# Performance work log

Measured on AMD Instinct MI355X. Metric: run time of the kernel, lower is better.

## Reference

```python
import jax, jax.numpy as jnp
import numpy as np

BATCH, D_MODEL, N_STATE, SEQ_L = 8, 1024, 64, 2048


def setup_inputs() -> dict:
    key = jax.random.key(0)
    k_u, k_a, k_b, k_c = jax.random.split(key, 4)
    scale = 1.0 / (D_MODEL * N_STATE) ** 0.5
    u = jax.random.normal(k_u, (BATCH, D_MODEL, SEQ_L), dtype=jnp.float32)
    # A is stored as a full NxN diagonal matrix, as in the torch module
    A = jnp.diag(jax.random.uniform(k_a, (N_STATE,), dtype=jnp.float32))
    B = jax.random.normal(k_b, (D_MODEL, N_STATE), dtype=jnp.float32) * scale
    C = jax.random.normal(k_c, (D_MODEL, N_STATE), dtype=jnp.float32) * scale
    return {"L": SEQ_L, "u": u, "A": A, "B": B, "C": C}


def reference(L, u, A, B, C):
    # u: (B, D, L). einsum('nn,bnd->bnd', A, h) in torch == diag(A) broadcast over h.
    a = jnp.diagonal(A)                       # (N,)
    Bu = jnp.einsum('dn,bdl->bnl', B, u)      # (B, N, L)
    Cu = jnp.einsum('dn,bdl->bnl', C, u)      # (B, N, L)
    bsz, d, _ = u.shape
    h0 = jnp.zeros((bsz, a.shape[0], d), dtype=u.dtype)  # (B, N, D)

    def step(h, xs):
        bu_l, cu_l, u_l = xs                  # (B,N), (B,N), (B,D)
        h = a[None, :, None] * h + bu_l[:, :, None] * u_l[:, None, :]
        y_l = jnp.einsum('bn,bnd->bd', cu_l, h)
        return h, y_l

    xs = (jnp.moveaxis(Bu, -1, 0), jnp.moveaxis(Cu, -1, 0), jnp.moveaxis(u, -1, 0))
    _, ys = jax.lax.scan(step, h0, xs)        # ys: (L, B, D)
    return jnp.moveaxis(ys, 0, -1)            # (B, D, L)
```

## Files before the change

kernel.cpp:

```cpp
#include <hip/hip_runtime.h>
#include <hip/hip_bf16.h>
#include <string.h>

#define BATCH 8
#define DM 1024
#define NS 64
#define SL 2048
#define NC 32
#define TC 64

typedef __attribute__((ext_vector_type(8))) short bf16x8;
typedef __attribute__((ext_vector_type(4))) float f32x4;
typedef float v2f __attribute__((ext_vector_type(2)));

__device__ inline unsigned short f2bf(float f) {
    union { float f; unsigned u; } v; v.f = f;
    return (unsigned short)((v.u + 0x7fffu + ((v.u >> 16) & 1u)) >> 16);
}
__device__ inline float bf2f(unsigned short h) {
    return __uint_as_float(((unsigned)h) << 16);
}
static __device__ inline v2f bfpair_to_v2f(unsigned int p) {
    unsigned int lo = p << 16, hi = p & 0xffff0000u;
    v2f r; r.x = __uint_as_float(lo); r.y = __uint_as_float(hi); return r;
}


__global__ __launch_bounds__(256) void k_prep(const float* __restrict__ Bm,
                                              const float* __restrict__ Cm,
                                              unsigned short* __restrict__ BT,
                                              unsigned short* __restrict__ CT)
{
    __shared__ float sT[64][65];
    const float* src = blockIdx.y ? Cm : Bm;
    unsigned short* dst = blockIdx.y ? CT : BT;
    const int d0 = blockIdx.x * 64, t = threadIdx.x;
    {
        int r = t >> 2, f = (t & 3) * 16;
#pragma unroll
        for (int i = 0; i < 4; i++) {
            float4 v = *(const float4*)&src[(size_t)(d0 + r) * NS + f + i * 4];
            sT[r][f + i * 4 + 0] = v.x; sT[r][f + i * 4 + 1] = v.y;
            sT[r][f + i * 4 + 2] = v.z; sT[r][f + i * 4 + 3] = v.w;
        }
    }
    __syncthreads();
    {
        int n = t >> 2, dq = (t & 3) * 16;
        unsigned pk[8];
#pragma unroll
        for (int k = 0; k < 8; k++) {
            unsigned short a = f2bf(sT[dq + 2 * k][n]);
            unsigned short bb = f2bf(sT[dq + 2 * k + 1][n]);
            pk[k] = (unsigned)a | ((unsigned)bb << 16);
        }
        uint4 v0 = { pk[0], pk[1], pk[2], pk[3] };
        uint4 v1 = { pk[4], pk[5], pk[6], pk[7] };
        *(uint4*)&dst[(size_t)n * DM + d0 + dq] = v0;
        *(uint4*)&dst[(size_t)n * DM + d0 + dq + 8] = v1;
    }
}

__global__ __launch_bounds__(512) void k_proj(const float* __restrict__ u,
                                              const unsigned short* __restrict__ BC,
                                              unsigned short* __restrict__ BuT,
                                              unsigned short* __restrict__ CuT,
                                              unsigned short* __restrict__ Ubf)
{
    __shared__ unsigned short sA[32 * 64];
    __shared__ unsigned short sB[128 * 64];
    const int b = blockIdx.y, l0 = blockIdx.x * 32, t = threadIdx.x;
    const int lane = t & 63, w = t >> 6, g = lane >> 4, m15 = lane & 15;
    const int dd = t >> 3, c8 = t & 7;
    const int dq = dd >> 3, d7 = dd & 7;

    f32x4 acc[2];
    acc[0] = (f32x4){0.f, 0.f, 0.f, 0.f};
    acc[1] = (f32x4){0.f, 0.f, 0.f, 0.f};

#pragma unroll 1
    for (int d0 = 0; d0 < DM; d0 += 64) {
        __syncthreads();
        {
            float4 v = *(const float4*)&u[((size_t)b * DM + d0 + dd) * SL + l0 + c8 * 4];
            unsigned short b0 = f2bf(v.x), b1 = f2bf(v.y), b2 = f2bf(v.z), b3 = f2bf(v.w);
            int l = c8 * 4;
            sA[(l + 0) * 64 + ((dq ^ ((l + 0) & 7)) * 8) + d7] = b0;
            sA[(l + 1) * 64 + ((dq ^ ((l + 1) & 7)) * 8) + d7] = b1;
            sA[(l + 2) * 64 + ((dq ^ ((l + 2) & 7)) * 8) + d7] = b2;
            sA[(l + 3) * 64 + ((dq ^ ((l + 3) & 7)) * 8) + d7] = b3;
            uint2 pk = { (unsigned)b0 | ((unsigned)b1 << 16),
                         (unsigned)b2 | ((unsigned)b3 << 16) };
            *(uint2*)(Ubf + ((size_t)b * DM + d0 + dd) * SL + l0 + c8 * 4) = pk;
        }
#pragma unroll
        for (int p = 0; p < 2; p++) {
            int idx = p * 512 + t;
            int row = idx >> 3, cc8 = idx & 7;
            uint4 v = *(const uint4*)(BC + (size_t)row * DM + d0 + cc8 * 8);
            *(uint4*)&sB[row * 64 + ((cc8 ^ (row & 7)) * 8)] = v;
        }
        __syncthreads();
#pragma unroll
        for (int ks = 0; ks < 2; ks++) {
            bf16x8 af[2], bfr;
#pragma unroll
            for (int mt = 0; mt < 2; mt++) {
                int r = mt * 16 + m15;
                af[mt] = *(const bf16x8*)&sA[r * 64 + (((ks * 4 + g) ^ (r & 7)) * 8)];
            }
            {
                int r = w * 16 + m15;
                bfr = *(const bf16x8*)&sB[r * 64 + (((ks * 4 + g) ^ (r & 7)) * 8)];
            }
#pragma unroll
            for (int mt = 0; mt < 2; mt++)
                acc[mt] = __builtin_amdgcn_mfma_f32_16x16x32_bf16(af[mt], bfr, acc[mt], 0, 0, 0);
        }
    }
    {
        int wn = w * 16 + m15;
        unsigned short* dst = (wn < 64) ? BuT : CuT;
        int n = wn & 63;
#pragma unroll
        for (int mt = 0; mt < 2; mt++)
#pragma unroll
            for (int r = 0; r < 4; r++) {
                int l = l0 + mt * 16 + g * 4 + r;
                dst[((size_t)b * SL + l) * NS + n] = f2bf(acc[mt][r]);
            }
    }
}

__global__ __launch_bounds__(256) void k_g(const float* __restrict__ A,
                                           const unsigned short* __restrict__ BuT,
                                           const unsigned short* __restrict__ CuT,
                                           unsigned short* __restrict__ Gw,
                                           unsigned short* __restrict__ Bvw,
                                           unsigned short* __restrict__ Wcw)
{
    __shared__ unsigned short sCu[64 * 64];
    __shared__ unsigned short sBu[8 * 64 * 8];
    __shared__ unsigned short sP[8 * 66 * 8];
    __shared__ unsigned short sTb[64 * 66];
    const int cc = blockIdx.x, b = cc >> 5, c = cc & 31;
    const int gy = blockIdx.y;
    const int t = threadIdx.x, lane = t & 63;
    const int l0 = c * TC;
    const size_t gbase = (size_t)cc * 4096;

    {
        const unsigned short* srcC = CuT + ((size_t)b * SL + l0) * NS;
        const unsigned short* srcB = BuT + ((size_t)b * SL + l0) * NS;
#pragma unroll
        for (int p = 0; p < 2; p++) {
            int idx = p * 256 + t;
            int r = idx >> 3, q8 = idx & 7;
            uint4 vc = *(const uint4*)(srcC + (size_t)r * NS + q8 * 8);
            *(uint4*)&sCu[r * 64 + q8 * 8] = vc;
            uint4 vb = *(const uint4*)(srcB + (size_t)r * NS + q8 * 8);
            *(uint4*)&sBu[(q8 * 64 + r) * 8] = vb;
        }
    }
    {
        int n = t & 63;
        float an = A[n * NS + n];
        int q = n >> 3, n7 = n & 7;
#pragma unroll 1
        for (int dl = (t >> 6) * 17; dl < (t >> 6) * 17 + 17 && dl <= 64; dl++)
            sP[(q * 66 + dl) * 8 + n7] = f2bf(__powf(an, (float)dl));
    }
    __syncthreads();

#pragma unroll 1
    for (int r = gy * 8; r < gy * 8 + 8; r++) {
        int idx = r * 256 + t;
        int l = idx >> 6;
        int lp = lane;
        int dl = l - lp;
        float acc = 0.f;
        if (dl >= 0) {
#pragma unroll
            for (int q = 0; q < 8; q++) {
                bf16x8 cu = *(const bf16x8*)&sCu[l * 64 + q * 8];
                bf16x8 bu = *(const bf16x8*)&sBu[(q * 64 + lp) * 8];
                bf16x8 pp = *(const bf16x8*)&sP[(q * 66 + dl) * 8];
#pragma unroll
                for (int j = 0; j < 8; j++)
                    acc = fmaf(bf2f((unsigned short)cu[j]) * bf2f((unsigned short)bu[j]),
                               bf2f((unsigned short)pp[j]), acc);
            }
        }
        Gw[gbase + l * 64 + lp] = (dl >= 0) ? f2bf(acc) : (unsigned short)0;
    }

    if (gy == 0) {
#pragma unroll 1
        for (int r = 0; r < 16; r++) {
            int idx = r * 256 + t;
            int l = idx >> 6;
            int n = lane, q = n >> 3, n7 = n & 7;
            float cu = bf2f(sCu[l * 64 + n]);
            float pv = bf2f(sP[(q * 66 + (l + 1)) * 8 + n7]);
            Wcw[gbase + l * 64 + n] = f2bf(cu * pv);
        }
    } else {
#pragma unroll 1
        for (int r = 0; r < 16; r++) {
            int idx = r * 256 + t;
            int l = idx >> 6;
            int n = lane, q = n >> 3, n7 = n & 7;
            float bu = bf2f(sBu[(q * 64 + l) * 8 + n7]);
            float pv = bf2f(sP[(q * 66 + (63 - l)) * 8 + n7]);
            sTb[n * 66 + l] = f2bf(bu * pv);
        }
        __syncthreads();
#pragma unroll 1
        for (int r = 0; r < 16; r++) {
            int idx = r * 256 + t;
            int n = idx >> 6;
            int l = lane;
            Bvw[gbase + n * 64 + l] = sTb[n * 66 + l];
        }
    }
}

__global__ __launch_bounds__(256) void k_state(const unsigned short* __restrict__ Ubf,
                                               const unsigned short* __restrict__ Bvw,
                                               unsigned short* __restrict__ Ew)
{
    __shared__ unsigned short sV[64 * 64];
    const int slab = blockIdx.x, c = blockIdx.y, b = blockIdx.z;
    const int d0 = slab * 128, l0 = c * TC;
    const int t = threadIdx.x, lane = t & 63, w = t >> 6, g = lane >> 4, m15 = lane & 15;

    {
        size_t gbase = ((size_t)(b * NC + c)) * 4096;
        int rr = t >> 3, c8 = t & 7;
#pragma unroll
        for (int p = 0; p < 2; p++) {
            int r = p * 32 + rr;
            uint4 vv = *(const uint4*)(Bvw + gbase + r * 64 + c8 * 8);
            *(uint4*)&sV[r * 64 + ((c8 ^ (r & 7)) * 8)] = vv;
        }
    }
    __syncthreads();

    const unsigned short* ub = Ubf + ((size_t)b * DM + d0) * SL + l0;

    f32x4 accE[2][4];
#pragma unroll
    for (int i = 0; i < 2; i++)
#pragma unroll
        for (int j = 0; j < 4; j++) accE[i][j] = (f32x4){0.f, 0.f, 0.f, 0.f};

#pragma unroll
    for (int ks = 0; ks < 2; ks++) {
        int kq = ks * 4 + g;
        bf16x8 af[2];
#pragma unroll
        for (int mt = 0; mt < 2; mt++) {
            int r = w * 32 + mt * 16 + m15;
            af[mt] = *(const bf16x8*)(ub + (size_t)r * SL + kq * 8);
        }
#pragma unroll
        for (int nt = 0; nt < 4; nt++) {
            int rg = nt * 16 + m15;
            bf16x8 bv = *(const bf16x8*)&sV[rg * 64 + ((kq ^ (rg & 7)) * 8)];
#pragma unroll
            for (int mt = 0; mt < 2; mt++)
                accE[mt][nt] = __builtin_amdgcn_mfma_f32_16x16x32_bf16(af[mt], bv, accE[mt][nt], 0, 0, 0);
        }
    }
#pragma unroll
    for (int mt = 0; mt < 2; mt++)
#pragma unroll
        for (int nt = 0; nt < 4; nt++)
#pragma unroll
            for (int r = 0; r < 4; r++) {
                int d = d0 + w * 32 + mt * 16 + g * 4 + r;
                Ew[(((size_t)b * NC + c) * DM + d) * NS + nt * 16 + m15] = f2bf(accE[mt][nt][r]);
            }
}

__global__ __launch_bounds__(256) void k_prefix(const float* __restrict__ A,
                                                unsigned short* __restrict__ E)
{
    int gg = blockIdx.x * 256 + threadIdx.x;
    int p  = gg & 31;
    int d  = (gg >> 5) & (DM - 1);
    int b  = gg >> 15;
    int n0 = p * 2;

    float a0 = A[n0 * NS + n0];
    float a1 = A[(n0 + 1) * NS + (n0 + 1)];
    v2f aT = { __powf(a0, (float)TC), __powf(a1, (float)TC) };
    v2f hs = { 0.f, 0.f };

    unsigned int* base = (unsigned int*)E + ((((size_t)b * NC) * DM + d) * NS >> 1) + p;
    const size_t cstride = ((size_t)DM * NS) >> 1;

#pragma unroll 4
    for (int c = 0; c < NC; c++) {
        unsigned int* ptr = base + (size_t)c * cstride;
        unsigned int e = *ptr;
        unsigned int sw = (unsigned)f2bf(hs.x) | ((unsigned)f2bf(hs.y) << 16);
        *ptr = sw;
        hs = __builtin_elementwise_fma(aT, hs, bfpair_to_v2f(e));
    }
}

__global__ __launch_bounds__(256) void k_y(const unsigned short* __restrict__ Ubf,
                                           const unsigned short* __restrict__ Gw,
                                           const unsigned short* __restrict__ Wcw,
                                           const unsigned short* __restrict__ HS,
                                           float* __restrict__ y)
{
    __shared__ unsigned short sG[64 * 64];
    __shared__ unsigned short sW[64 * 64];
    const int slab = blockIdx.x, c = blockIdx.y, b = blockIdx.z;
    const int d0 = slab * 128, l0 = c * TC;
    const int t = threadIdx.x, lane = t & 63, w = t >> 6, g = lane >> 4, m15 = lane & 15;

    {
        size_t gbase = ((size_t)(b * NC + c)) * 4096;
        int rr = t >> 3, c8 = t & 7;
#pragma unroll
        for (int p = 0; p < 2; p++) {
            int r = p * 32 + rr;
            uint4 gv = *(const uint4*)(Gw + gbase + r * 64 + c8 * 8);
            *(uint4*)&sG[r * 64 + ((c8 ^ (r & 7)) * 8)] = gv;
            uint4 wv = *(const uint4*)(Wcw + gbase + r * 64 + c8 * 8);
            *(uint4*)&sW[r * 64 + ((c8 ^ (r & 7)) * 8)] = wv;
        }
    }
    __syncthreads();

    const unsigned short* ub    = Ubf + ((size_t)b * DM + d0) * SL + l0;
    const unsigned short* hbase = HS + (((size_t)b * NC + c) * DM + d0) * NS;

    f32x4 acc[2][4];
#pragma unroll
    for (int i = 0; i < 2; i++)
#pragma unroll
        for (int j = 0; j < 4; j++) acc[i][j] = (f32x4){0.f, 0.f, 0.f, 0.f};

#pragma unroll
    for (int ks = 0; ks < 2; ks++) {
        int kq = ks * 4 + g;
        bf16x8 af[2];
#pragma unroll
        for (int mt = 0; mt < 2; mt++) {
            int r = w * 32 + mt * 16 + m15;
            af[mt] = *(const bf16x8*)(ub + (size_t)r * SL + kq * 8);
        }
#pragma unroll
        for (int nt = 0; nt < 4; nt++) {
            int rg = nt * 16 + m15;
            bf16x8 bg = *(const bf16x8*)&sG[rg * 64 + ((kq ^ (rg & 7)) * 8)];
#pragma unroll
            for (int mt = 0; mt < 2; mt++)
                acc[mt][nt] = __builtin_amdgcn_mfma_f32_16x16x32_bf16(af[mt], bg, acc[mt][nt], 0, 0, 0);
        }
    }
#pragma unroll
    for (int ks = 0; ks < 2; ks++) {
        int kq = ks * 4 + g;
        bf16x8 ah[2];
#pragma unroll
        for (int mt = 0; mt < 2; mt++) {
            int r = w * 32 + mt * 16 + m15;
            ah[mt] = *(const bf16x8*)(hbase + (size_t)r * NS + kq * 8);
        }
#pragma unroll
        for (int nt = 0; nt < 4; nt++) {
            int rg = nt * 16 + m15;
            bf16x8 bw = *(const bf16x8*)&sW[rg * 64 + ((kq ^ (rg & 7)) * 8)];
#pragma unroll
            for (int mt = 0; mt < 2; mt++)
                acc[mt][nt] = __builtin_amdgcn_mfma_f32_16x16x32_bf16(ah[mt], bw, acc[mt][nt], 0, 0, 0);
        }
    }
#pragma unroll
    for (int mt = 0; mt < 2; mt++)
#pragma unroll
        for (int nt = 0; nt < 4; nt++)
#pragma unroll
            for (int r = 0; r < 4; r++) {
                int d = d0 + w * 32 + mt * 16 + g * 4 + r;
                int l = l0 + nt * 16 + m15;
                y[((size_t)b * DM + d) * SL + l] = acc[mt][nt][r];
            }
}

extern "C" void kernel_launch(void* const* d_in, const int* in_sizes, int n_in,
                              void* d_out, int out_size, void* d_ws, size_t ws_size,
                              hipStream_t stream) {
    const float* u = (const float*)d_in[1];
    const float* A = (const float*)d_in[2];
    const float* B = (const float*)d_in[3];
    const float* C = (const float*)d_in[4];
    float* y = (float*)d_out;

    char* base = (char*)d_ws;
    unsigned short* BuT = (unsigned short*)(base);
    unsigned short* CuT = (unsigned short*)(base + (2u << 20));
    unsigned short* BT  = (unsigned short*)(base + (4u << 20));
    unsigned short* Gw  = (unsigned short*)(base + (5u << 20));
    unsigned short* Bvw = (unsigned short*)(base + (7u << 20));
    unsigned short* Wcw = (unsigned short*)(base + (9u << 20));
    unsigned short* Ew  = (unsigned short*)(base + (11u << 20));
    unsigned short* Ubf = (unsigned short*)(base + (44u << 20));
    unsigned short* CT  = BT + (size_t)NS * DM;

    k_prep<<<dim3(DM / 64, 2), 256, 0, stream>>>(B, C, BT, CT);
    k_proj<<<dim3(SL / 32, BATCH), 512, 0, stream>>>(u, BT, BuT, CuT, Ubf);
    k_g<<<dim3(BATCH * NC, 2), 256, 0, stream>>>(A, BuT, CuT, Gw, Bvw, Wcw);
    k_state<<<dim3(8, NC, BATCH), 256, 0, stream>>>(Ubf, Bvw, Ew);
    k_prefix<<<dim3(BATCH * DM * 32 / 256), 256, 0, stream>>>(A, Ew);
    k_y<<<dim3(8, NC, BATCH), 256, 0, stream>>>(Ubf, Gw, Wcw, Ew, y);
}
```

Baseline: 108.1 us.

## Split k_proj reduction over D into two halves with fp32 partials

The projection kernel now splits the 1024-wide D reduction across two blocks along a new grid z dimension. Each block writes fp32 partial sums to a workspace buffer, and k_g adds the two partials before rounding to bf16. This doubles the number of blocks for the projection GEMM (512 to 1024) to fill more CUs and shortens each block's serial loop. In exchange it adds more intermediate traffic (fp32 and two copies) and a larger workspace layout.

```diff
diff --git a/kernel.cpp b/kernel.cpp
--- a/kernel.cpp
+++ b/kernel.cpp
@@ -63,13 +63,12 @@
 
 __global__ __launch_bounds__(512) void k_proj(const float* __restrict__ u,
                                               const unsigned short* __restrict__ BC,
-                                              unsigned short* __restrict__ BuT,
-                                              unsigned short* __restrict__ CuT,
+                                              float* __restrict__ P,
                                               unsigned short* __restrict__ Ubf)
 {
     __shared__ unsigned short sA[32 * 64];
     __shared__ unsigned short sB[128 * 64];
-    const int b = blockIdx.y, l0 = blockIdx.x * 32, t = threadIdx.x;
+    const int b = blockIdx.y, l0 = blockIdx.x * 32, kk = blockIdx.z, t = threadIdx.x;
     const int lane = t & 63, w = t >> 6, g = lane >> 4, m15 = lane & 15;
     const int dd = t >> 3, c8 = t & 7;
     const int dq = dd >> 3, d7 = dd & 7;
@@ -79,7 +78,8 @@
     acc[1] = (f32x4){0.f, 0.f, 0.f, 0.f};
 
 #pragma unroll 1
-    for (int d0 = 0; d0 < DM; d0 += 64) {
+    for (int it = 0; it < 8; it++) {
+        const int d0 = (kk << 9) + it * 64;
         __syncthreads();
         {
             float4 v = *(const float4*)&u[((size_t)b * DM + d0 + dd) * SL + l0 + c8 * 4];
@@ -120,21 +120,19 @@
     }
     {
         int wn = w * 16 + m15;
-        unsigned short* dst = (wn < 64) ? BuT : CuT;
-        int n = wn & 63;
+        float* dst = P + ((size_t)(kk * BATCH + b) * SL) * 128;
 #pragma unroll
         for (int mt = 0; mt < 2; mt++)
 #pragma unroll
             for (int r = 0; r < 4; r++) {
                 int l = l0 + mt * 16 + g * 4 + r;
-                dst[((size_t)b * SL + l) * NS + n] = f2bf(acc[mt][r]);
+                dst[(size_t)l * 128 + wn] = acc[mt][r];
             }
     }
 }
 
 __global__ __launch_bounds__(256) void k_g(const float* __restrict__ A,
-                                           const unsigned short* __restrict__ BuT,
-                                           const unsigned short* __restrict__ CuT,
+                                           const float* __restrict__ P,
                                            unsigned short* __restrict__ Gw,
                                            unsigned short* __restrict__ Bvw,
                                            unsigned short* __restrict__ Wcw)
@@ -150,16 +148,34 @@
     const size_t gbase = (size_t)cc * 4096;
 
     {
-        const unsigned short* srcC = CuT + ((size_t)b * SL + l0) * NS;
-        const unsigned short* srcB = BuT + ((size_t)b * SL + l0) * NS;
+        const float* p0 = P + ((size_t)b * SL + l0) * 128;
+        const float* p1 = P + ((size_t)(BATCH + b) * SL + l0) * 128;
 #pragma unroll
         for (int p = 0; p < 2; p++) {
             int idx = p * 256 + t;
             int r = idx >> 3, q8 = idx & 7;
-            uint4 vc = *(const uint4*)(srcC + (size_t)r * NS + q8 * 8);
+            const float* r0 = p0 + (size_t)r * 128;
+            const float* r1 = p1 + (size_t)r * 128;
+            float4 a0 = *(const float4*)&r0[q8 * 8];
+            float4 a1 = *(const float4*)&r0[q8 * 8 + 4];
+            float4 b0 = *(const float4*)&r1[q8 * 8];
+            float4 b1 = *(const float4*)&r1[q8 * 8 + 4];
+            uint4 vb;
+            vb.x = (unsigned)f2bf(a0.x + b0.x) | ((unsigned)f2bf(a0.y + b0.y) << 16);
+            vb.y = (unsigned)f2bf(a0.z + b0.z) | ((unsigned)f2bf(a0.w + b0.w) << 16);
+            vb.z = (unsigned)f2bf(a1.x + b1.x) | ((unsigned)f2bf(a1.y + b1.y) << 16);
+            vb.w = (unsigned)f2bf(a1.z + b1.z) | ((unsigned)f2bf(a1.w + b1.w) << 16);
+            *(uint4*)&sBu[(q8 * 64 + r) * 8] = vb;
+            float4 c0 = *(const float4*)&r0[64 + q8 * 8];
+            float4 c1 = *(const float4*)&r0[64 + q8 * 8 + 4];
+            float4 d0v = *(const float4*)&r1[64 + q8 * 8];
+            float4 d1v = *(const float4*)&r1[64 + q8 * 8 + 4];
+            uint4 vc;
+            vc.x = (unsigned)f2bf(c0.x + d0v.x) | ((unsigned)f2bf(c0.y + d0v.y) << 16);
+            vc.y = (unsigned)f2bf(c0.z + d0v.z) | ((unsigned)f2bf(c0.w + d0v.w) << 16);
+            vc.z = (unsigned)f2bf(c1.x + d1v.x) | ((unsigned)f2bf(c1.y + d1v.y) << 16);
+            vc.w = (unsigned)f2bf(c1.z + d1v.z) | ((unsigned)f2bf(c1.w + d1v.w) << 16);
             *(uint4*)&sCu[r * 64 + q8 * 8] = vc;
-            uint4 vb = *(const uint4*)(srcB + (size_t)r * NS + q8 * 8);
-            *(uint4*)&sBu[(q8 * 64 + r) * 8] = vb;
         }
     }
     {
@@ -403,19 +419,18 @@
     float* y = (float*)d_out;
 
     char* base = (char*)d_ws;
-    unsigned short* BuT = (unsigned short*)(base);
-    unsigned short* CuT = (unsigned short*)(base + (2u << 20));
-    unsigned short* BT  = (unsigned short*)(base + (4u << 20));
-    unsigned short* Gw  = (unsigned short*)(base + (5u << 20));
-    unsigned short* Bvw = (unsigned short*)(base + (7u << 20));
-    unsigned short* Wcw = (unsigned short*)(base + (9u << 20));
-    unsigned short* Ew  = (unsigned short*)(base + (11u << 20));
-    unsigned short* Ubf = (unsigned short*)(base + (44u << 20));
+    float*          Pp  = (float*)(base);
+    unsigned short* BT  = (unsigned short*)(base + (16u << 20));
+    unsigned short* Gw  = (unsigned short*)(base + (17u << 20));
+    unsigned short* Bvw = (unsigned short*)(base + (19u << 20));
+    unsigned short* Wcw = (unsigned short*)(base + (21u << 20));
+    unsigned short* Ew  = (unsigned short*)(base + (24u << 20));
+    unsigned short* Ubf = (unsigned short*)(base + (56u << 20));
     unsigned short* CT  = BT + (size_t)NS * DM;
 
     k_prep<<<dim3(DM / 64, 2), 256, 0, stream>>>(B, C, BT, CT);
-    k_proj<<<dim3(SL / 32, BATCH), 512, 0, stream>>>(u, BT, BuT, CuT, Ubf);
-    k_g<<<dim3(BATCH * NC, 2), 256, 0, stream>>>(A, BuT, CuT, Gw, Bvw, Wcw);
+    k_proj<<<dim3(SL / 32, BATCH, 2), 512, 0, stream>>>(u, BT, Pp, Ubf);
+    k_g<<<dim3(BATCH * NC, 2), 256, 0, stream>>>(A, Pp, Gw, Bvw, Wcw);
     k_state<<<dim3(8, NC, BATCH), 256, 0, stream>>>(Ubf, Bvw, Ew);
     k_prefix<<<dim3(BATCH * DM * 32 / 256), 256, 0, stream>>>(A, Ew);
     k_y<<<dim3(8, NC, BATCH), 256, 0, stream>>>(Ubf, Gw, Wcw, Ew, y);
```

After: 111.6 us. 3.3% more time.

## Split-K the projection GEMM into fp32 partials reduced in k_g

Applied to the files above, without the earlier changes.

The projection kernel now splits the D_MODEL reduction into four slices across a new grid dimension. Each block uses 256 threads with a 2x2 MFMA tile per wave and writes fp32 partial sums to a workspace buffer. The consumer kernel k_g sums the four partials and converts them to bf16 when loading its chunk. This trades a shorter serial K-loop and more blocks for an extra 32 MB fp32 partial buffer that is written and read back.

```diff
diff --git a/kernel.cpp b/kernel.cpp
--- a/kernel.cpp
+++ b/kernel.cpp
@@ -8,6 +8,7 @@
 #define SL 2048
 #define NC 32
 #define TC 64
+#define KK 4
 
 typedef __attribute__((ext_vector_type(8))) short bf16x8;
 typedef __attribute__((ext_vector_type(4))) float f32x4;
@@ -61,27 +62,31 @@
     }
 }
 
-__global__ __launch_bounds__(512) void k_proj(const float* __restrict__ u,
+__global__ __launch_bounds__(256) void k_proj(const float* __restrict__ u,
                                               const unsigned short* __restrict__ BC,
-                                              unsigned short* __restrict__ BuT,
-                                              unsigned short* __restrict__ CuT,
+                                              float* __restrict__ P,
                                               unsigned short* __restrict__ Ubf)
 {
     __shared__ unsigned short sA[32 * 64];
     __shared__ unsigned short sB[128 * 64];
-    const int b = blockIdx.y, l0 = blockIdx.x * 32, t = threadIdx.x;
+    const int b = blockIdx.y, l0 = blockIdx.x * 32, kk = blockIdx.z, t = threadIdx.x;
     const int lane = t & 63, w = t >> 6, g = lane >> 4, m15 = lane & 15;
-    const int dd = t >> 3, c8 = t & 7;
-    const int dq = dd >> 3, d7 = dd & 7;
-
-    f32x4 acc[2];
-    acc[0] = (f32x4){0.f, 0.f, 0.f, 0.f};
-    acc[1] = (f32x4){0.f, 0.f, 0.f, 0.f};
-
-#pragma unroll 1
-    for (int d0 = 0; d0 < DM; d0 += 64) {
+
+    f32x4 acc[2][2];
+#pragma unroll
+    for (int i = 0; i < 2; i++)
+#pragma unroll
+        for (int j = 0; j < 2; j++) acc[i][j] = (f32x4){0.f, 0.f, 0.f, 0.f};
+
+#pragma unroll 1
+    for (int it = 0; it < 4; it++) {
+        const int d0 = (kk << 8) + it * 64;
         __syncthreads();
-        {
+#pragma unroll
+        for (int p = 0; p < 2; p++) {
+            int idx = p * 256 + t;
+            int dd = idx >> 3, c8 = idx & 7;
+            int dq = dd >> 3, d7 = dd & 7;
             float4 v = *(const float4*)&u[((size_t)b * DM + d0 + dd) * SL + l0 + c8 * 4];
             unsigned short b0 = f2bf(v.x), b1 = f2bf(v.y), b2 = f2bf(v.z), b3 = f2bf(v.w);
             int l = c8 * 4;
@@ -94,8 +99,8 @@
             *(uint2*)(Ubf + ((size_t)b * DM + d0 + dd) * SL + l0 + c8 * 4) = pk;
         }
 #pragma unroll
-        for (int p = 0; p < 2; p++) {
-            int idx = p * 512 + t;
+        for (int p = 0; p < 4; p++) {
+            int idx = p * 256 + t;
             int row = idx >> 3, cc8 = idx & 7;
             uint4 v = *(const uint4*)(BC + (size_t)row * DM + d0 + cc8 * 8);
             *(uint4*)&sB[row * 64 + ((cc8 ^ (row & 7)) * 8)] = v;
@@ -103,38 +108,43 @@
         __syncthreads();
 #pragma unroll
         for (int ks = 0; ks < 2; ks++) {
-            bf16x8 af[2], bfr;
+            int kq = ks * 4 + g;
+            bf16x8 af[2], bfr[2];
 #pragma unroll
             for (int mt = 0; mt < 2; mt++) {
                 int r = mt * 16 + m15;
-                af[mt] = *(const bf16x8*)&sA[r * 64 + (((ks * 4 + g) ^ (r & 7)) * 8)];
-            }
-            {
-                int r = w * 16 + m15;
-                bfr = *(const bf16x8*)&sB[r * 64 + (((ks * 4 + g) ^ (r & 7)) * 8)];
+                af[mt] = *(const bf16x8*)&sA[r * 64 + ((kq ^ (r & 7)) * 8)];
+            }
+#pragma unroll
+            for (int nt = 0; nt < 2; nt++) {
+                int r = w * 32 + nt * 16 + m15;
+                bfr[nt] = *(const bf16x8*)&sB[r * 64 + ((kq ^ (r & 7)) * 8)];
             }
 #pragma unroll
             for (int mt = 0; mt < 2; mt++)
-                acc[mt] = __builtin_amdgcn_mfma_f32_16x16x32_bf16(af[mt], bfr, acc[mt], 0, 0, 0);
-        }
-    }
-    {
-        int wn = w * 16 + m15;
-        unsigned short* dst = (wn < 64) ? BuT : CuT;
-        int n = wn & 63;
+#pragma unroll
+                for (int nt = 0; nt < 2; nt++)
+                    acc[mt][nt] = __builtin_amdgcn_mfma_f32_16x16x32_bf16(af[mt], bfr[nt], acc[mt][nt], 0, 0, 0);
+        }
+    }
+    {
+        float* dst = P + ((size_t)(kk * BATCH + b) * SL) * 128;
 #pragma unroll
         for (int mt = 0; mt < 2; mt++)
 #pragma unroll
-            for (int r = 0; r < 4; r++) {
-                int l = l0 + mt * 16 + g * 4 + r;
-                dst[((size_t)b * SL + l) * NS + n] = f2bf(acc[mt][r]);
+            for (int nt = 0; nt < 2; nt++) {
+                int wn = w * 32 + nt * 16 + m15;
+#pragma unroll
+                for (int r = 0; r < 4; r++) {
+                    int l = l0 + mt * 16 + g * 4 + r;
+                    dst[(size_t)l * 128 + wn] = acc[mt][nt][r];
+                }
             }
     }
 }
 
 __global__ __launch_bounds__(256) void k_g(const float* __restrict__ A,
-                                           const unsigned short* __restrict__ BuT,
-                                           const unsigned short* __restrict__ CuT,
+                                           const float* __restrict__ P,
                                            unsigned short* __restrict__ Gw,
                                            unsigned short* __restrict__ Bvw,
                                            unsigned short* __restrict__ Wcw)
@@ -150,16 +160,36 @@
     const size_t gbase = (size_t)cc * 4096;
 
     {
-        const unsigned short* srcC = CuT + ((size_t)b * SL + l0) * NS;
-        const unsigned short* srcB = BuT + ((size_t)b * SL + l0) * NS;
 #pragma unroll
         for (int p = 0; p < 2; p++) {
             int idx = p * 256 + t;
             int r = idx >> 3, q8 = idx & 7;
-            uint4 vc = *(const uint4*)(srcC + (size_t)r * NS + q8 * 8);
+            float sb[8], sc[8];
+#pragma unroll
+            for (int j = 0; j < 8; j++) { sb[j] = 0.f; sc[j] = 0.f; }
+#pragma unroll
+            for (int kk = 0; kk < KK; kk++) {
+                const float* rp = P + ((size_t)(kk * BATCH + b) * SL + l0 + r) * 128;
+                float4 a0 = *(const float4*)&rp[q8 * 8];
+                float4 a1 = *(const float4*)&rp[q8 * 8 + 4];
+                sb[0] += a0.x; sb[1] += a0.y; sb[2] += a0.z; sb[3] += a0.w;
+                sb[4] += a1.x; sb[5] += a1.y; sb[6] += a1.z; sb[7] += a1.w;
+                float4 c0 = *(const float4*)&rp[64 + q8 * 8];
+                float4 c1 = *(const float4*)&rp[64 + q8 * 8 + 4];
+                sc[0] += c0.x; sc[1] += c0.y; sc[2] += c0.z; sc[3] += c0.w;
+                sc[4] += c1.x; sc[5] += c1.y; sc[6] += c1.z; sc[7] += c1.w;
+            }
+            uint4 vb, vc;
+            vb.x = (unsigned)f2bf(sb[0]) | ((unsigned)f2bf(sb[1]) << 16);
+            vb.y = (unsigned)f2bf(sb[2]) | ((unsigned)f2bf(sb[3]) << 16);
+            vb.z = (unsigned)f2bf(sb[4]) | ((unsigned)f2bf(sb[5]) << 16);
+            vb.w = (unsigned)f2bf(sb[6]) | ((unsigned)f2bf(sb[7]) << 16);
+            *(uint4*)&sBu[(q8 * 64 + r) * 8] = vb;
+            vc.x = (unsigned)f2bf(sc[0]) | ((unsigned)f2bf(sc[1]) << 16);
+            vc.y = (unsigned)f2bf(sc[2]) | ((unsigned)f2bf(sc[3]) << 16);
+            vc.z = (unsigned)f2bf(sc[4]) | ((unsigned)f2bf(sc[5]) << 16);
+            vc.w = (unsigned)f2bf(sc[6]) | ((unsigned)f2bf(sc[7]) << 16);
             *(uint4*)&sCu[r * 64 + q8 * 8] = vc;
-            uint4 vb = *(const uint4*)(srcB + (size_t)r * NS + q8 * 8);
-            *(uint4*)&sBu[(q8 * 64 + r) * 8] = vb;
         }
     }
     {
@@ -403,19 +433,18 @@
     float* y = (float*)d_out;
 
     char* base = (char*)d_ws;
-    unsigned short* BuT = (unsigned short*)(base);
-    unsigned short* CuT = (unsigned short*)(base + (2u << 20));
-    unsigned short* BT  = (unsigned short*)(base + (4u << 20));
-    unsigned short* Gw  = (unsigned short*)(base + (5u << 20));
-    unsigned short* Bvw = (unsigned short*)(base + (7u << 20));
-    unsigned short* Wcw = (unsigned short*)(base + (9u << 20));
-    unsigned short* Ew  = (unsigned short*)(base + (11u << 20));
-    unsigned short* Ubf = (unsigned short*)(base + (44u << 20));
+    float*          Pp  = (float*)(base);
+    unsigned short* BT  = (unsigned short*)(base + (32u << 20));
+    unsigned short* Gw  = (unsigned short*)(base + (33u << 20));
+    unsigned short* Bvw = (unsigned short*)(base + (35u << 20));
+    unsigned short* Wcw = (unsigned short*)(base + (37u << 20));
+    unsigned short* Ew  = (unsigned short*)(base + (40u << 20));
+    unsigned short* Ubf = (unsigned short*)(base + (72u << 20));
     unsigned short* CT  = BT + (size_t)NS * DM;
 
     k_prep<<<dim3(DM / 64, 2), 256, 0, stream>>>(B, C, BT, CT);
-    k_proj<<<dim3(SL / 32, BATCH), 512, 0, stream>>>(u, BT, BuT, CuT, Ubf);
-    k_g<<<dim3(BATCH * NC, 2), 256, 0, stream>>>(A, BuT, CuT, Gw, Bvw, Wcw);
+    k_proj<<<dim3(SL / 32, BATCH, KK), 256, 0, stream>>>(u, BT, Pp, Ubf);
+    k_g<<<dim3(BATCH * NC, 2), 256, 0, stream>>>(A, Pp, Gw, Bvw, Wcw);
     k_state<<<dim3(8, NC, BATCH), 256, 0, stream>>>(Ubf, Bvw, Ew);
     k_prefix<<<dim3(BATCH * DM * 32 / 256), 256, 0, stream>>>(A, Ew);
     k_y<<<dim3(8, NC, BATCH), 256, 0, stream>>>(Ubf, Gw, Wcw, Ew, y);
```

Result: slower. 115.9 us (+7.3%).
